# Kernel tuning notes

Hardware: AMD Instinct MI355X
Metric: run time of the kernel (lower is better)

## Reference

```python
import jax, jax.numpy as jnp
from jax import lax
import numpy as np

H = 512
W = 512
SIGMA = 0.1
IN_CH = [3, 66, 64, 64, 32, 32, 32, 16, 16]
OUT_CH = [64, 64, 64, 32, 32, 32, 16, 16, 16]
N_LAYERS = 9


def setup_inputs() -> dict:
    key = jax.random.key(0)
    ks = jax.random.split(key, 32)
    inp = {}
    inp['x'] = jax.random.uniform(ks[0], (3, 3, 1, 1), jnp.float32)  # query + 2 neighbor coords
    inp['neighbors'] = jax.random.uniform(ks[1], (2, 3, H, W), jnp.float32)
    inp['albedo_index'] = 4
    for i in range(N_LAYERS):
        kh = 1 if i == 0 else 3
        fan_in = IN_CH[i] * kh * kh
        inp[f'w{i}'] = jax.random.normal(ks[2 + i], (OUT_CH[i], IN_CH[i], kh, kh), jnp.float32) / np.sqrt(fan_in).astype(np.float32)
        inp[f'b{i}'] = jnp.zeros((OUT_CH[i],), jnp.float32)
    inp['wf'] = jax.random.normal(ks[20], (6, 16, 3, 3), jnp.float32) / np.sqrt(16 * 9).astype(np.float32)
    inp['bf'] = jnp.zeros((6,), jnp.float32)
    inp['albedos'] = 0.5 + jax.random.uniform(ks[21], (9, 3, H, W), jnp.float32)
    return inp


def _conv(x, w, b):
    y = lax.conv_general_dilated(x, w, (1, 1), 'VALID', dimension_numbers=('NCHW', 'OIHW', 'NCHW'))
    return y + b[None, :, None, None]


def _decoder(x, ws, bs, wf, bf):
    # coordconv constant [[ [0,2],[0,2] ], [ [0,0],[2,2] ]] with shape [2,2,2]
    coordconv = jnp.array([[[0., 2.], [0., 2.]], [[0., 0.], [2., 2.]]], dtype=x.dtype)
    for i in range(N_LAYERS):
        x = jnp.repeat(jnp.repeat(x, 2, axis=2), 2, axis=3)  # nearest upsample x2
        if i > 0:
            x = jnp.pad(x, ((0, 0), (0, 0), (1, 1), (1, 1)), mode='reflect')
        x = jax.nn.leaky_relu(_conv(x, ws[i], bs[i]), 0.01)
        if i == 0:
            cc = jnp.broadcast_to(coordconv[None], (x.shape[0],) + coordconv.shape)
            x = jnp.concatenate([x, cc], axis=1)  # -> 66 channels at 2x2
    x = jnp.pad(x, ((0, 0), (0, 0), (1, 1), (1, 1)), mode='reflect')
    return jnp.tanh(_conv(x, wf, bf))  # [B, 6, H, W]


def _grid_sample_border(img, grid):
    # bilinear, padding_mode='border', align_corners=False (matches torch grid_sample)
    N, C, Hh, Ww = img.shape
    gx = jnp.clip((grid[..., 0] + 1.0) * Ww / 2.0 - 0.5, 0.0, Ww - 1.0)
    gy = jnp.clip((grid[..., 1] + 1.0) * Hh / 2.0 - 0.5, 0.0, Hh - 1.0)
    x0 = jnp.floor(gx)
    y0 = jnp.floor(gy)
    wx = (gx - x0)[:, None]  # [N,1,H,W]
    wy = (gy - y0)[:, None]
    x0i = jnp.clip(x0.astype(jnp.int32), 0, Ww - 1)
    x1i = jnp.clip(x0i + 1, 0, Ww - 1)
    y0i = jnp.clip(y0.astype(jnp.int32), 0, Hh - 1)
    y1i = jnp.clip(y0i + 1, 0, Hh - 1)
    g = jax.vmap(lambda im, yi, xi: im[:, yi, xi])
    v00 = g(img, y0i, x0i)
    v01 = g(img, y0i, x1i)
    v10 = g(img, y1i, x0i)
    v11 = g(img, y1i, x1i)
    return v00 * (1 - wx) * (1 - wy) + v01 * wx * (1 - wy) + v10 * (1 - wx) * wy + v11 * wx * wy


def _blending(x, neighbors, flows, albedo):
    eps = 1e-5
    light_flow, view_flow, time_flow = flows[:1, 0:2], flows[:1, 2:4], flows[:1, 4:6]
    lf_n, vf_n, tf_n = flows[1:, 0:2], flows[1:, 2:4], flows[1:, 4:6]
    delta = x[:1] - x[1:]  # [2,3,1,1], broadcasts in place of torch.tile
    dl, dv, dt = delta[:, 0:1], delta[:, 1:2], delta[:, 2:3]
    flag = (jnp.abs(dl) > 0).astype(flows.dtype)
    offset_fwd = dl * light_flow + dv * view_flow + dt * time_flow  # [2,2,H,W]
    shading = flag * neighbors / albedo + (1 - flag) * neighbors
    ys = jnp.linspace(-1.0, 1.0, H)
    xs = jnp.linspace(-1.0, 1.0, W)
    grid_base = jnp.stack(jnp.meshgrid(xs, ys, indexing='xy'), axis=-1)  # [H,W,2], (...,0)=x
    grid = grid_base[None] + offset_fwd.transpose(0, 2, 3, 1)  # [2,H,W,2]
    warped_shading = _grid_sample_border(shading, grid)
    warped_vf = _grid_sample_border(vf_n, grid)
    warped_tf = _grid_sample_border(tf_n, grid)
    warped_lf = _grid_sample_border(lf_n, grid)
    warped_image = flag * warped_shading * albedo + (1 - flag) * warped_shading
    offset_bwd = dl * warped_lf + dv * warped_vf + dt * warped_tf
    dist = jnp.sum(jnp.abs(offset_fwd - offset_bwd), axis=1, keepdims=True)
    weight = jnp.exp(-SIGMA * W * dist)
    wn = weight / (jnp.sum(weight, axis=0, keepdims=True) + eps)
    return jnp.sum(warped_image * wn, axis=0, keepdims=True)  # [1,3,H,W]


def reference(x, neighbors, albedo_index, w0, w1, w2, w3, w4, w5, w6, w7, w8,
              b0, b1, b2, b3, b4, b5, b6, b7, b8, wf, bf, albedos):
    ws = [w0, w1, w2, w3, w4, w5, w6, w7, w8]
    bs = [b0, b1, b2, b3, b4, b5, b6, b7, b8]
    flows = _decoder(x, ws, bs, wf, bf)
    albedo = albedos[albedo_index]  # [3,H,W]
    return _blending(x, neighbors, flows, albedo)
```

## Files before the change

kernel.cpp:

```cpp
#include <hip/hip_runtime.h>
#include <hip/hip_bf16.h>
#include <math.h>


#define HH 512
#define WWI 512
#define HWP (HH*WWI)

__global__ void k_layer0(const float* __restrict__ xin, const float* __restrict__ w,
                         const float* __restrict__ bias, float* __restrict__ out)
{
  for (int idx = threadIdx.x; idx < 3*66*4; idx += blockDim.x) {
    int pos = idx & 3;
    int c = (idx >> 2) % 66;
    int b = idx / (66*4);
    float v;
    if (c < 64) {
      float a = bias[c];
      #pragma unroll
      for (int ci = 0; ci < 3; ci++) a += w[c*3+ci] * xin[b*3+ci];
      v = (a >= 0.f) ? a : 0.01f*a;
    } else {
      int xx = pos & 1, yy = pos >> 1;
      v = (c == 64) ? 2.f*(float)xx : 2.f*(float)yy;
    }
    out[idx] = v;
  }
}

__device__ __forceinline__ int refl_up(int t, int n) {
  t = (t < 0) ? -t : t;
  t = (t >= n) ? (2*(n-1) - t) : t;
  return t >> 1;
}

template<int G>
__global__ void k_conv_lds(const float* __restrict__ in, float* __restrict__ out,
                           const float* __restrict__ w, const float* __restrict__ bias,
                           int B, int Cin, int CO, int COB, int Hin, int TR, int SPAN)
{
  extern __shared__ float lds[];
  const int Hout = Hin * 2;
  const int rowTiles = Hout / TR;
  const int coTiles = CO / COB;
  int bid = blockIdx.x;
  int tile = bid % rowTiles;
  int cot  = (bid / rowTiles) % coTiles;
  int b    = bid / (rowTiles * coTiles);
  int tr0  = tile * TR;
  int co_base = cot * COB;

  int r0 = tr0/2 - 1;
  if (r0 < 0) r0 = 0;
  if (r0 > Hin - SPAN) r0 = Hin - SPAN;

  float* wlds = lds;
  float* blds = wlds + COB*Cin*9;
  float* ilds = blds + COB;

  int nt = blockDim.x, tid = threadIdx.x;

  const float* wsrc = w + (size_t)co_base*Cin*9;
  for (int i = tid; i < COB*Cin*9; i += nt) wlds[i] = wsrc[i];
  for (int i = tid; i < COB; i += nt) blds[i] = bias[co_base + i];
  int icount = Cin*SPAN*Hin;
  for (int i = tid; i < icount; i += nt) {
    int col = i % Hin;
    int r = (i / Hin) % SPAN;
    int ci = i / (Hin*SPAN);
    ilds[i] = in[(((size_t)b*Cin + ci)*Hin + (r0 + r))*Hin + col];
  }
  __syncthreads();

  int npix = TR * Hout;
  int ngr = COB / G;
  int items = ngr * npix;
  for (int it = tid; it < items; it += nt) {
    int pix = it % npix;
    int cg = it / npix;
    int x = pix % Hout;
    int y = tr0 + pix / Hout;

    int ry[3], rx[3];
    #pragma unroll
    for (int d = 0; d < 3; d++) {
      int s = refl_up(y - 1 + d, Hout) - r0;
      s = (s < 0) ? 0 : s;
      s = (s > SPAN-1) ? SPAN-1 : s;
      ry[d] = s;
      rx[d] = refl_up(x - 1 + d, Hout);
    }

    float acc[G];
    #pragma unroll
    for (int j = 0; j < G; j++) acc[j] = blds[cg*G + j];

    for (int ci = 0; ci < Cin; ci++) {
      const float* ib = ilds + (size_t)ci*SPAN*Hin;
      float p[9];
      #pragma unroll
      for (int dy = 0; dy < 3; dy++)
        #pragma unroll
        for (int dx = 0; dx < 3; dx++)
          p[dy*3+dx] = ib[ry[dy]*Hin + rx[dx]];
      const float* wc = wlds + ((size_t)(cg*G)*Cin + ci)*9;
      #pragma unroll
      for (int j = 0; j < G; j++) {
        #pragma unroll
        for (int k = 0; k < 9; k++) acc[j] += wc[(size_t)j*Cin*9 + k] * p[k];
      }
    }

    #pragma unroll
    for (int j = 0; j < G; j++) {
      float v = acc[j];
      v = (v >= 0.f) ? v : 0.01f*v;
      out[(((size_t)b*CO + co_base + cg*G + j)*Hout + y)*Hout + x] = v;
    }
  }
}

__global__ void k_foldw6(const float* __restrict__ w3, const float* __restrict__ w4,
                         const float* __restrict__ w5, const float* __restrict__ w6,
                         const float* __restrict__ w7, const float* __restrict__ w8,
                         float* __restrict__ f3, float* __restrict__ f4,
                         float* __restrict__ f5, float* __restrict__ f6,
                         float* __restrict__ f7, float* __restrict__ f8)
{
  int idx = blockIdx.x*blockDim.x + threadIdx.x;
  const float* w; float* f; int n;
  if      (idx < 2048) { w = w3; f = f3; n = idx; }
  else if (idx < 3072) { w = w4; f = f4; n = idx - 2048; }
  else if (idx < 4096) { w = w5; f = f5; n = idx - 3072; }
  else if (idx < 4608) { w = w6; f = f6; n = idx - 4096; }
  else if (idx < 4864) { w = w7; f = f7; n = idx - 4608; }
  else if (idx < 5120) { w = w8; f = f8; n = idx - 4864; }
  else return;

  const float* ws = w + (size_t)n*9;
  float W[9];
  #pragma unroll
  for (int k = 0; k < 9; k++) W[k] = ws[k];

  float a[2][2][3];
  #pragma unroll
  for (int c = 0; c < 3; c++) {
    a[0][0][c] = W[c];          a[0][1][c] = W[3+c] + W[6+c];
    a[1][0][c] = W[c] + W[3+c]; a[1][1][c] = W[6+c];
  }
  float* fo = f + (size_t)n*16;
  #pragma unroll
  for (int py = 0; py < 2; py++)
    #pragma unroll
    for (int px = 0; px < 2; px++) {
      int p = py*2 + px;
      #pragma unroll
      for (int ky = 0; ky < 2; ky++) {
        float kx0 = (px == 0) ? a[py][ky][0] : (a[py][ky][0] + a[py][ky][1]);
        float kx1 = (px == 0) ? (a[py][ky][1] + a[py][ky][2]) : a[py][ky][2];
        fo[p*4 + ky*2 + 0] = kx0;
        fo[p*4 + ky*2 + 1] = kx1;
      }
    }
}

__global__ void k_upconv_s(const float* __restrict__ in, float* __restrict__ out,
                           const float* __restrict__ wfold, const float* __restrict__ bias,
                           int B, int Cin, int CO, int Hin)
{
  extern __shared__ float4 wlds4[];
  int nt = blockDim.x, tid = threadIdx.x;
  int co = blockIdx.y;
  int stride = Cin + 1;
  const float4* wsrc = reinterpret_cast<const float4*>(wfold);
  for (int s = tid; s < Cin*4; s += nt) {
    int p = s & 3;
    int ci = s >> 2;
    wlds4[p*stride + ci] = wsrc[(size_t)(co*Cin + ci)*4 + p];
  }
  __syncthreads();

  int Hout = Hin * 2;
  int npix = B * Hout * Hout;
  int idx = blockIdx.x*nt + tid;
  if (idx >= npix) return;
  int x = idx % Hout;
  int y = (idx / Hout) % Hout;
  int b = idx / (Hout * Hout);

  int X = x >> 1, Y = y >> 1;
  int px = x & 1, py = y & 1;

  int r_lo = py ? Y : (Y > 0 ? Y-1 : 0);
  int r_hi = py ? (Y < Hin-1 ? Y+1 : Hin-1) : Y;
  int c_lo = px ? X : (X > 0 ? X-1 : 0);
  int c_hi = px ? (X < Hin-1 ? X+1 : Hin-1) : X;

  float acc = bias[co];

  const size_t plane = (size_t)Hin * Hin;
  const float* ibase = in + (size_t)b * Cin * plane;
  const float4* wb = wlds4 + (py*2 + px) * stride;

  for (int ci = 0; ci < Cin; ci++) {
    const float* ip = ibase + (size_t)ci * plane;
    const float* rl = ip + (size_t)r_lo * Hin;
    const float* rh = ip + (size_t)r_hi * Hin;
    float4 w4 = wb[ci];
    acc += w4.x*rl[c_lo] + w4.y*rl[c_hi] + w4.z*rh[c_lo] + w4.w*rh[c_hi];
  }

  float v = (acc >= 0.f) ? acc : 0.01f*acc;
  out[((size_t)b*CO + co)*((size_t)Hout*Hout) + (size_t)y*Hout + x] = v;
}

template<int CO>
__global__ void k_upconv_w(const float* __restrict__ in, float* __restrict__ out,
                           const float* __restrict__ wfold, const float* __restrict__ bias,
                           int B, int Cin, int Hin)
{
  extern __shared__ float4 wlds4[];
  int nt = blockDim.x, tid = threadIdx.x;
  int stride = Cin * CO + 1;
  int nw = Cin * CO * 4;
  const float4* wsrc = reinterpret_cast<const float4*>(wfold);
  for (int s = tid; s < nw; s += nt) {
    int p = s & 3;
    int r = s >> 2;
    int ci = r % Cin;
    int co = r / Cin;
    wlds4[p*stride + ci*CO + co] = wsrc[s];
  }
  __syncthreads();

  int Hout = Hin * 2;
  int total = B * Hout * Hout;
  int idx = blockIdx.x*nt + tid;
  if (idx >= total) return;
  int x = idx % Hout;
  int y = (idx / Hout) % Hout;
  int b = idx / (Hout * Hout);

  int X = x >> 1, Y = y >> 1;
  int px = x & 1, py = y & 1;

  int r_lo = py ? Y : (Y > 0 ? Y-1 : 0);
  int r_hi = py ? (Y < Hin-1 ? Y+1 : Hin-1) : Y;
  int c_lo = px ? X : (X > 0 ? X-1 : 0);
  int c_hi = px ? (X < Hin-1 ? X+1 : Hin-1) : X;

  float acc[CO];
  #pragma unroll
  for (int co = 0; co < CO; co++) acc[co] = bias[co];

  const size_t plane = (size_t)Hin * Hin;
  const float* ibase = in + (size_t)b * Cin * plane;
  const float4* wb = wlds4 + (py*2 + px) * stride;

  for (int ci = 0; ci < Cin; ci++) {
    const float* ip = ibase + (size_t)ci * plane;
    const float* rl = ip + (size_t)r_lo * Hin;
    const float* rh = ip + (size_t)r_hi * Hin;
    float p00 = rl[c_lo], p01 = rl[c_hi];
    float p10 = rh[c_lo], p11 = rh[c_hi];

    const float4* wc = wb + ci * CO;
    #pragma unroll
    for (int co = 0; co < CO; co++) {
      float4 w4 = wc[co];
      acc[co] += w4.x*p00 + w4.y*p01 + w4.z*p10 + w4.w*p11;
    }
  }

  int pix = y*Hout + x;
  #pragma unroll
  for (int co = 0; co < CO; co++) {
    float v = acc[co];
    v = (v >= 0.f) ? v : 0.01f*v;
    out[((size_t)b*CO + co)*((size_t)Hout*Hout) + pix] = v;
  }
}

template<int CO>
__global__ void k_upconv_w2(const float* __restrict__ in, float* __restrict__ out,
                            const float* __restrict__ wfold, const float* __restrict__ bias,
                            int B, int Cin, int Hin)
{
  extern __shared__ float4 wlds4[];
  int nt = blockDim.x, tid = threadIdx.x;
  int stride = Cin * CO + 1;
  int nw = Cin * CO * 4;
  const float4* wsrc = reinterpret_cast<const float4*>(wfold);
  for (int s = tid; s < nw; s += nt) {
    int p = s & 3;
    int r = s >> 2;
    int ci = r % Cin;
    int co = r / Cin;
    wlds4[p*stride + ci*CO + co] = wsrc[s];
  }
  __syncthreads();

  int Hout = Hin * 2;
  int half = Hout >> 1;
  int total = B * Hout * half;
  int idx = blockIdx.x*nt + tid;
  if (idx >= total) return;
  int x1 = idx % half;
  int y  = (idx / half) % Hout;
  int b  = idx / (half * Hout);

  int px = x1 & 1, py = y & 1;
  int X1 = x1 >> 1, Y = y >> 1;
  int X2 = X1 + (Hin >> 1);

  int r_lo = py ? Y : (Y > 0 ? Y-1 : 0);
  int r_hi = py ? (Y < Hin-1 ? Y+1 : Hin-1) : Y;
  int c1lo = px ? X1 : (X1 > 0 ? X1-1 : 0);
  int c1hi = px ? (X1 < Hin-1 ? X1+1 : Hin-1) : X1;
  int c2lo = px ? X2 : (X2 > 0 ? X2-1 : 0);
  int c2hi = px ? (X2 < Hin-1 ? X2+1 : Hin-1) : X2;

  float acc0[CO], acc1[CO];
  #pragma unroll
  for (int co = 0; co < CO; co++) { float bv = bias[co]; acc0[co] = bv; acc1[co] = bv; }

  const size_t plane = (size_t)Hin * Hin;
  const float* ibase = in + (size_t)b * Cin * plane;
  const float4* wb = wlds4 + (py*2 + px) * stride;

  for (int ci = 0; ci < Cin; ci++) {
    const float* ip = ibase + (size_t)ci * plane;
    const float* rl = ip + (size_t)r_lo * Hin;
    const float* rh = ip + (size_t)r_hi * Hin;
    float a0 = rl[c1lo], a1 = rl[c1hi];
    float a2 = rh[c1lo], a3 = rh[c1hi];
    float b0 = rl[c2lo], b1 = rl[c2hi];
    float b2 = rh[c2lo], b3 = rh[c2hi];

    const float4* wc = wb + ci * CO;
    #pragma unroll
    for (int co = 0; co < CO; co++) {
      float4 w4 = wc[co];
      acc0[co] += w4.x*a0 + w4.y*a1 + w4.z*a2 + w4.w*a3;
      acc1[co] += w4.x*b0 + w4.y*b1 + w4.z*b2 + w4.w*b3;
    }
  }

  size_t oplane = (size_t)Hout * Hout;
  size_t pix1 = (size_t)y*Hout + x1;
  float* obase = out + (size_t)b * CO * oplane;
  #pragma unroll
  for (int co = 0; co < CO; co++) {
    float v0 = acc0[co]; v0 = (v0 >= 0.f) ? v0 : 0.01f*v0;
    float v1 = acc1[co]; v1 = (v1 >= 0.f) ? v1 : 0.01f*v1;
    float* op = obase + (size_t)co * oplane;
    op[pix1] = v0;
    op[pix1 + half] = v1;
  }
}

__global__ void k_final(const float* __restrict__ in, float* __restrict__ out,
                        const float* __restrict__ w, const float* __restrict__ bias)
{
  int idx = blockIdx.x*blockDim.x + threadIdx.x;
  int total = 3 * HWP;
  if (idx >= total) return;
  int x = idx & (WWI-1);
  int y = (idx >> 9) & (HH-1);
  int b = idx / HWP;

  int ry[3], rx[3];
  #pragma unroll
  for (int d = 0; d < 3; d++) {
    int t = y - 1 + d;
    t = (t < 0) ? -t : t;
    ry[d] = (t >= HH) ? (2*(HH-1) - t) : t;
    t = x - 1 + d;
    t = (t < 0) ? -t : t;
    rx[d] = (t >= WWI) ? (2*(WWI-1) - t) : t;
  }

  float acc[6];
  #pragma unroll
  for (int co = 0; co < 6; co++) acc[co] = bias[co];

  for (int ci = 0; ci < 16; ci++) {
    const float* ib = in + ((size_t)(b*16) + ci) * HWP;
    float p[9];
    #pragma unroll
    for (int dy = 0; dy < 3; dy++)
      #pragma unroll
      for (int dx = 0; dx < 3; dx++)
        p[dy*3+dx] = ib[ry[dy]*WWI + rx[dx]];
    const float* wc = w + ci*9;
    #pragma unroll
    for (int co = 0; co < 6; co++) {
      const float* wcc = wc + co*16*9;
      #pragma unroll
      for (int k = 0; k < 9; k++) acc[co] += wcc[k] * p[k];
    }
  }

  int pix = y*WWI + x;
  #pragma unroll
  for (int co = 0; co < 6; co++)
    out[((size_t)(b*6) + co)*HWP + pix] = tanhf(acc[co]);
}

__global__ void k_blend(const float* __restrict__ xin, const float* __restrict__ neighbors,
                        const int* __restrict__ aidx, const float* __restrict__ albedos,
                        const float* __restrict__ flows, float* __restrict__ out)
{
  int idx = blockIdx.x*blockDim.x + threadIdx.x;
  if (idx >= HWP) return;
  int xo = idx & (WWI-1);
  int yo = idx >> 9;

  float xv[9];
  #pragma unroll
  for (int i = 0; i < 9; i++) xv[i] = xin[i];

  float f0[6];
  #pragma unroll
  for (int c = 0; c < 6; c++) f0[c] = flows[(size_t)c*HWP + idx];

  const float* alb = albedos + (size_t)aidx[0]*3*HWP;
  float albp[3];
  #pragma unroll
  for (int ch = 0; ch < 3; ch++) albp[ch] = alb[(size_t)ch*HWP + idx];

  float num0 = 0.f, num1 = 0.f, num2 = 0.f;
  float wsum = 0.f;

  #pragma unroll
  for (int n = 0; n < 2; n++) {
    float dl = xv[0] - xv[(n+1)*3 + 0];
    float dv = xv[1] - xv[(n+1)*3 + 1];
    float dt = xv[2] - xv[(n+1)*3 + 2];
    bool fl = fabsf(dl) > 0.f;

    float ofx = dl*f0[0] + dv*f0[2] + dt*f0[4];
    float ofy = dl*f0[1] + dv*f0[3] + dt*f0[5];

    float gx = ((-1.f + (2.f/511.f)*(float)xo) + ofx + 1.f)*256.f - 0.5f;
    float gy = ((-1.f + (2.f/511.f)*(float)yo) + ofy + 1.f)*256.f - 0.5f;
    gx = fminf(fmaxf(gx, 0.f), 511.f);
    gy = fminf(fmaxf(gy, 0.f), 511.f);

    float x0f = floorf(gx), y0f = floorf(gy);
    float wx = gx - x0f, wy = gy - y0f;
    int x0i = (int)x0f, y0i = (int)y0f;
    int x1i = min(x0i + 1, WWI-1), y1i = min(y0i + 1, HH-1);

    float cw[4] = {(1.f-wx)*(1.f-wy), wx*(1.f-wy), (1.f-wx)*wy, wx*wy};
    int   cp[4] = {y0i*WWI + x0i, y0i*WWI + x1i, y1i*WWI + x0i, y1i*WWI + x1i};

    const float* nb = neighbors + (size_t)n*3*HWP;
    const float* Fn = flows + (size_t)(n+1)*6*HWP;

    float s0=0.f,s1=0.f,s2=0.f;
    float l0=0.f,l1=0.f,v0=0.f,v1=0.f,t0=0.f,t1=0.f;
    #pragma unroll
    for (int c = 0; c < 4; c++) {
      int p = cp[c];
      float ww = cw[c];
      float n0 = nb[p];
      float n1 = nb[HWP + p];
      float n2 = nb[2*HWP + p];
      if (fl) {
        n0 /= alb[p];
        n1 /= alb[HWP + p];
        n2 /= alb[2*HWP + p];
      }
      s0 += ww*n0; s1 += ww*n1; s2 += ww*n2;
      l0 += ww*Fn[p];             l1 += ww*Fn[HWP + p];
      v0 += ww*Fn[2*HWP + p];     v1 += ww*Fn[3*HWP + p];
      t0 += ww*Fn[4*HWP + p];     t1 += ww*Fn[5*HWP + p];
    }

    float wi0 = fl ? s0*albp[0] : s0;
    float wi1 = fl ? s1*albp[1] : s1;
    float wi2 = fl ? s2*albp[2] : s2;

    float obx = dl*l0 + dv*v0 + dt*t0;
    float oby = dl*l1 + dv*v1 + dt*t1;
    float dist = fabsf(ofx - obx) + fabsf(ofy - oby);
    float wgt = expf(-51.2f * dist);

    wsum += wgt;
    num0 += wgt*wi0; num1 += wgt*wi1; num2 += wgt*wi2;
  }

  float inv = 1.f / (wsum + 1e-5f);
  out[idx]         = num0*inv;
  out[HWP + idx]   = num1*inv;
  out[2*HWP + idx] = num2*inv;
}

extern "C" void kernel_launch(void* const* d_in, const int* in_sizes, int n_in,
                              void* d_out, int out_size, void* d_ws, size_t ws_size,
                              hipStream_t stream) {
  const float* x         = (const float*)d_in[0];
  const float* neighbors = (const float*)d_in[1];
  const int*   aidx      = (const int*)d_in[2];
  const float* wts[10];
  const float* bis[10];
  for (int i = 0; i < 9; i++) { wts[i] = (const float*)d_in[3+2*i]; bis[i] = (const float*)d_in[4+2*i]; }
  wts[9] = (const float*)d_in[21];
  bis[9] = (const float*)d_in[22];
  const float* albedos = (const float*)d_in[23];

  float* wk   = (float*)d_ws;
  float* bufS = wk;
  float* bufA = wk + 800;
  float* bufB = bufA + 4718592;
  size_t need = (size_t)(800 + 4718592 + 12582912) * 4;
  if (ws_size < need) return;

  float* wf3 = bufA + 3200000;
  float* wf4 = wf3 + 32768;
  float* wf5 = wf4 + 16384;
  float* wf6 = wf5 + 16384;
  float* wf7 = wf6 + 8192;
  float* wf8 = wf7 + 4096;
  k_foldw6<<<20, 256, 0, stream>>>(wts[3], wts[4], wts[5], wts[6], wts[7], wts[8],
                                   wf3, wf4, wf5, wf6, wf7, wf8);

  k_layer0<<<1, 256, 0, stream>>>(x, wts[0], bis[0], bufS);

  auto spanOf = [](int Hin, int TR) { int s = TR/2 + 2; return (s > Hin) ? Hin : s; };
  auto ldsB = [&](int COB, int Cin, int Hin, int TR) {
    return (size_t)(COB*Cin*9 + COB + Cin*spanOf(Hin,TR)*Hin) * 4;
  };

  k_conv_lds<1><<<48, 256, ldsB(4,66,2,4), stream>>>(bufS, bufA, wts[1], bis[1],
                                                     3, 66, 64, 4, 2, 4, spanOf(2,4));
  k_conv_lds<1><<<96, 256, ldsB(2,64,4,8), stream>>>(bufA, bufB, wts[2], bis[2],
                                                     3, 64, 64, 2, 4, 8, spanOf(4,8));
  {
    dim3 g3(3*16*16/256, 32), g4(3*32*32/256, 32), g5(3*64*64/256, 32);
    k_upconv_s<<<g3, 256, (size_t)4*(64+1)*16, stream>>>(bufB, bufA, wf3, bis[3], 3, 64, 32, 8);
    k_upconv_s<<<g4, 256, (size_t)4*(32+1)*16, stream>>>(bufA, bufB, wf4, bis[4], 3, 32, 32, 16);
    k_upconv_s<<<g5, 256, (size_t)4*(32+1)*16, stream>>>(bufB, bufA, wf5, bis[5], 3, 32, 32, 32);
  }

  auto blocks = [](int total){ return (total + 255) / 256; };
  k_upconv_w<16><<<blocks(3*128*128), 256, (size_t)4*(32*16+1)*16, stream>>>(bufA, bufB, wf6, bis[6], 3, 32, 64);
  k_upconv_w2<16><<<blocks(3*256*128), 256, (size_t)4*(16*16+1)*16, stream>>>(bufB, bufA, wf7, bis[7], 3, 16, 128);
  k_upconv_w2<16><<<blocks(3*512*256), 256, (size_t)4*(16*16+1)*16, stream>>>(bufA, bufB, wf8, bis[8], 3, 16, 256);

  k_final<<<blocks(3*HWP), 256, 0, stream>>>(bufB, bufA, wts[9], bis[9]);
  k_blend<<<blocks(HWP), 256, 0, stream>>>(x, neighbors, aidx, albedos, bufA, (float*)d_out);
}
```

Measured before the change: 332.2 us.

## Fold layers 1-2 into upconv, split layer 8 by channel, two-pixel final conv

Layers 1 and 2 now use the same pre-folded 2x2 upsample-conv weights as the later layers, run through the folded small-layer kernel, which removes the generic LDS conv kernel. The layer-8 upconv is split across two output-channel halves per block to cut register pressure and add parallelism. The final 3x3 conv computes two adjacent pixels per thread, sharing the loaded neighbourhood and writing float2. The fold kernel grows to cover eight layers, and the channel split for layer 8 reads each input twice.

Result: faster. 321.2 us (-3.3%).

```diff
diff --git a/kernel.cpp b/kernel.cpp
--- a/kernel.cpp
+++ b/kernel.cpp
@@ -28,113 +28,25 @@
   }
 }
 
-__device__ __forceinline__ int refl_up(int t, int n) {
-  t = (t < 0) ? -t : t;
-  t = (t >= n) ? (2*(n-1) - t) : t;
-  return t >> 1;
-}
-
-template<int G>
-__global__ void k_conv_lds(const float* __restrict__ in, float* __restrict__ out,
-                           const float* __restrict__ w, const float* __restrict__ bias,
-                           int B, int Cin, int CO, int COB, int Hin, int TR, int SPAN)
-{
-  extern __shared__ float lds[];
-  const int Hout = Hin * 2;
-  const int rowTiles = Hout / TR;
-  const int coTiles = CO / COB;
-  int bid = blockIdx.x;
-  int tile = bid % rowTiles;
-  int cot  = (bid / rowTiles) % coTiles;
-  int b    = bid / (rowTiles * coTiles);
-  int tr0  = tile * TR;
-  int co_base = cot * COB;
-
-  int r0 = tr0/2 - 1;
-  if (r0 < 0) r0 = 0;
-  if (r0 > Hin - SPAN) r0 = Hin - SPAN;
-
-  float* wlds = lds;
-  float* blds = wlds + COB*Cin*9;
-  float* ilds = blds + COB;
-
-  int nt = blockDim.x, tid = threadIdx.x;
-
-  const float* wsrc = w + (size_t)co_base*Cin*9;
-  for (int i = tid; i < COB*Cin*9; i += nt) wlds[i] = wsrc[i];
-  for (int i = tid; i < COB; i += nt) blds[i] = bias[co_base + i];
-  int icount = Cin*SPAN*Hin;
-  for (int i = tid; i < icount; i += nt) {
-    int col = i % Hin;
-    int r = (i / Hin) % SPAN;
-    int ci = i / (Hin*SPAN);
-    ilds[i] = in[(((size_t)b*Cin + ci)*Hin + (r0 + r))*Hin + col];
-  }
-  __syncthreads();
-
-  int npix = TR * Hout;
-  int ngr = COB / G;
-  int items = ngr * npix;
-  for (int it = tid; it < items; it += nt) {
-    int pix = it % npix;
-    int cg = it / npix;
-    int x = pix % Hout;
-    int y = tr0 + pix / Hout;
-
-    int ry[3], rx[3];
-    #pragma unroll
-    for (int d = 0; d < 3; d++) {
-      int s = refl_up(y - 1 + d, Hout) - r0;
-      s = (s < 0) ? 0 : s;
-      s = (s > SPAN-1) ? SPAN-1 : s;
-      ry[d] = s;
-      rx[d] = refl_up(x - 1 + d, Hout);
-    }
-
-    float acc[G];
-    #pragma unroll
-    for (int j = 0; j < G; j++) acc[j] = blds[cg*G + j];
-
-    for (int ci = 0; ci < Cin; ci++) {
-      const float* ib = ilds + (size_t)ci*SPAN*Hin;
-      float p[9];
-      #pragma unroll
-      for (int dy = 0; dy < 3; dy++)
-        #pragma unroll
-        for (int dx = 0; dx < 3; dx++)
-          p[dy*3+dx] = ib[ry[dy]*Hin + rx[dx]];
-      const float* wc = wlds + ((size_t)(cg*G)*Cin + ci)*9;
-      #pragma unroll
-      for (int j = 0; j < G; j++) {
-        #pragma unroll
-        for (int k = 0; k < 9; k++) acc[j] += wc[(size_t)j*Cin*9 + k] * p[k];
-      }
-    }
-
-    #pragma unroll
-    for (int j = 0; j < G; j++) {
-      float v = acc[j];
-      v = (v >= 0.f) ? v : 0.01f*v;
-      out[(((size_t)b*CO + co_base + cg*G + j)*Hout + y)*Hout + x] = v;
-    }
-  }
-}
-
-__global__ void k_foldw6(const float* __restrict__ w3, const float* __restrict__ w4,
+__global__ void k_foldw8(const float* __restrict__ w1, const float* __restrict__ w2,
+                         const float* __restrict__ w3, const float* __restrict__ w4,
                          const float* __restrict__ w5, const float* __restrict__ w6,
                          const float* __restrict__ w7, const float* __restrict__ w8,
+                         float* __restrict__ f1, float* __restrict__ f2,
                          float* __restrict__ f3, float* __restrict__ f4,
                          float* __restrict__ f5, float* __restrict__ f6,
                          float* __restrict__ f7, float* __restrict__ f8)
 {
   int idx = blockIdx.x*blockDim.x + threadIdx.x;
   const float* w; float* f; int n;
-  if      (idx < 2048) { w = w3; f = f3; n = idx; }
-  else if (idx < 3072) { w = w4; f = f4; n = idx - 2048; }
-  else if (idx < 4096) { w = w5; f = f5; n = idx - 3072; }
-  else if (idx < 4608) { w = w6; f = f6; n = idx - 4096; }
-  else if (idx < 4864) { w = w7; f = f7; n = idx - 4608; }
-  else if (idx < 5120) { w = w8; f = f8; n = idx - 4864; }
+  if      (idx < 4224)  { w = w1; f = f1; n = idx; }
+  else if (idx < 8320)  { w = w2; f = f2; n = idx - 4224; }
+  else if (idx < 10368) { w = w3; f = f3; n = idx - 8320; }
+  else if (idx < 11392) { w = w4; f = f4; n = idx - 10368; }
+  else if (idx < 12416) { w = w5; f = f5; n = idx - 11392; }
+  else if (idx < 12928) { w = w6; f = f6; n = idx - 12416; }
+  else if (idx < 13184) { w = w7; f = f7; n = idx - 12928; }
+  else if (idx < 13440) { w = w8; f = f8; n = idx - 13184; }
   else return;
 
   const float* ws = w + (size_t)n*9;
@@ -281,22 +193,23 @@
   }
 }
 
-template<int CO>
-__global__ void k_upconv_w2(const float* __restrict__ in, float* __restrict__ out,
-                            const float* __restrict__ wfold, const float* __restrict__ bias,
-                            int B, int Cin, int Hin)
+template<int COB>
+__global__ void k_upconv_w2c(const float* __restrict__ in, float* __restrict__ out,
+                             const float* __restrict__ wfold, const float* __restrict__ bias,
+                             int B, int Cin, int CO, int Hin)
 {
   extern __shared__ float4 wlds4[];
   int nt = blockDim.x, tid = threadIdx.x;
-  int stride = Cin * CO + 1;
-  int nw = Cin * CO * 4;
+  int co0 = blockIdx.y * COB;
+  int stride = Cin * COB + 1;
+  int nw = Cin * COB * 4;
   const float4* wsrc = reinterpret_cast<const float4*>(wfold);
   for (int s = tid; s < nw; s += nt) {
     int p = s & 3;
     int r = s >> 2;
     int ci = r % Cin;
-    int co = r / Cin;
-    wlds4[p*stride + ci*CO + co] = wsrc[s];
+    int col = r / Cin;
+    wlds4[p*stride + ci*COB + col] = wsrc[(size_t)((co0 + col)*Cin + ci)*4 + p];
   }
   __syncthreads();
 
@@ -320,9 +233,9 @@
   int c2lo = px ? X2 : (X2 > 0 ? X2-1 : 0);
   int c2hi = px ? (X2 < Hin-1 ? X2+1 : Hin-1) : X2;
 
-  float acc0[CO], acc1[CO];
-  #pragma unroll
-  for (int co = 0; co < CO; co++) { float bv = bias[co]; acc0[co] = bv; acc1[co] = bv; }
+  float acc0[COB], acc1[COB];
+  #pragma unroll
+  for (int j = 0; j < COB; j++) { float bv = bias[co0 + j]; acc0[j] = bv; acc1[j] = bv; }
 
   const size_t plane = (size_t)Hin * Hin;
   const float* ibase = in + (size_t)b * Cin * plane;
@@ -337,74 +250,87 @@
     float b0 = rl[c2lo], b1 = rl[c2hi];
     float b2 = rh[c2lo], b3 = rh[c2hi];
 
-    const float4* wc = wb + ci * CO;
-    #pragma unroll
-    for (int co = 0; co < CO; co++) {
-      float4 w4 = wc[co];
-      acc0[co] += w4.x*a0 + w4.y*a1 + w4.z*a2 + w4.w*a3;
-      acc1[co] += w4.x*b0 + w4.y*b1 + w4.z*b2 + w4.w*b3;
+    const float4* wc = wb + ci * COB;
+    #pragma unroll
+    for (int j = 0; j < COB; j++) {
+      float4 w4 = wc[j];
+      acc0[j] += w4.x*a0 + w4.y*a1 + w4.z*a2 + w4.w*a3;
+      acc1[j] += w4.x*b0 + w4.y*b1 + w4.z*b2 + w4.w*b3;
     }
   }
 
   size_t oplane = (size_t)Hout * Hout;
   size_t pix1 = (size_t)y*Hout + x1;
-  float* obase = out + (size_t)b * CO * oplane;
-  #pragma unroll
-  for (int co = 0; co < CO; co++) {
-    float v0 = acc0[co]; v0 = (v0 >= 0.f) ? v0 : 0.01f*v0;
-    float v1 = acc1[co]; v1 = (v1 >= 0.f) ? v1 : 0.01f*v1;
-    float* op = obase + (size_t)co * oplane;
+  float* op = out + ((size_t)b * CO + co0) * oplane;
+  #pragma unroll
+  for (int j = 0; j < COB; j++) {
+    float v0 = acc0[j]; v0 = (v0 >= 0.f) ? v0 : 0.01f*v0;
+    float v1 = acc1[j]; v1 = (v1 >= 0.f) ? v1 : 0.01f*v1;
     op[pix1] = v0;
     op[pix1 + half] = v1;
-  }
-}
-
-__global__ void k_final(const float* __restrict__ in, float* __restrict__ out,
-                        const float* __restrict__ w, const float* __restrict__ bias)
+    op += oplane;
+  }
+}
+
+__global__ void k_final2(const float* __restrict__ in, float* __restrict__ out,
+                         const float* __restrict__ w, const float* __restrict__ bias)
 {
   int idx = blockIdx.x*blockDim.x + threadIdx.x;
-  int total = 3 * HWP;
+  int total = 3 * HH * (WWI/2);
   if (idx >= total) return;
-  int x = idx & (WWI-1);
-  int y = (idx >> 9) & (HH-1);
-  int b = idx / HWP;
-
-  int ry[3], rx[3];
+  int xh = idx % (WWI/2);
+  int y  = (idx / (WWI/2)) % HH;
+  int b  = idx / (HH * (WWI/2));
+  int x0 = 2*xh;
+
+  int ry[3];
   #pragma unroll
   for (int d = 0; d < 3; d++) {
     int t = y - 1 + d;
     t = (t < 0) ? -t : t;
     ry[d] = (t >= HH) ? (2*(HH-1) - t) : t;
-    t = x - 1 + d;
-    t = (t < 0) ? -t : t;
-    rx[d] = (t >= WWI) ? (2*(WWI-1) - t) : t;
-  }
-
-  float acc[6];
-  #pragma unroll
-  for (int co = 0; co < 6; co++) acc[co] = bias[co];
+  }
+  int cx[4];
+  cx[0] = (x0 == 0) ? 1 : x0-1;
+  cx[1] = x0;
+  cx[2] = x0+1;
+  cx[3] = (x0+2 >= WWI) ? (2*(WWI-1) - (x0+2)) : x0+2;
+
+  float acc0[6], acc1[6];
+  #pragma unroll
+  for (int co = 0; co < 6; co++) { float bv = bias[co]; acc0[co] = bv; acc1[co] = bv; }
 
   for (int ci = 0; ci < 16; ci++) {
     const float* ib = in + ((size_t)(b*16) + ci) * HWP;
-    float p[9];
-    #pragma unroll
-    for (int dy = 0; dy < 3; dy++)
+    float p[3][4];
+    #pragma unroll
+    for (int dy = 0; dy < 3; dy++) {
+      const float* r = ib + (size_t)ry[dy]*WWI;
       #pragma unroll
-      for (int dx = 0; dx < 3; dx++)
-        p[dy*3+dx] = ib[ry[dy]*WWI + rx[dx]];
+      for (int dx = 0; dx < 4; dx++) p[dy][dx] = r[cx[dx]];
+    }
     const float* wc = w + ci*9;
     #pragma unroll
     for (int co = 0; co < 6; co++) {
       const float* wcc = wc + co*16*9;
       #pragma unroll
-      for (int k = 0; k < 9; k++) acc[co] += wcc[k] * p[k];
-    }
-  }
-
-  int pix = y*WWI + x;
-  #pragma unroll
-  for (int co = 0; co < 6; co++)
-    out[((size_t)(b*6) + co)*HWP + pix] = tanhf(acc[co]);
+      for (int dy = 0; dy < 3; dy++) {
+        #pragma unroll
+        for (int dx = 0; dx < 3; dx++) {
+          float wv = wcc[dy*3+dx];
+          acc0[co] += wv * p[dy][dx];
+          acc1[co] += wv * p[dy][dx+1];
+        }
+      }
+    }
+  }
+
+  size_t pix = (size_t)y*WWI + x0;
+  #pragma unroll
+  for (int co = 0; co < 6; co++) {
+    float2 v = make_float2(tanhf(acc0[co]), tanhf(acc1[co]));
+    *reinterpret_cast<float2*>(out + ((size_t)(b*6) + co)*HWP + pix) = v;
+  }
 }
 
 __global__ void k_blend(const float* __restrict__ xin, const float* __restrict__ neighbors,
@@ -517,38 +443,41 @@
   size_t need = (size_t)(800 + 4718592 + 12582912) * 4;
   if (ws_size < need) return;
 
-  float* wf3 = bufA + 3200000;
+  float* wf1 = bufA + 3200000;
+  float* wf2 = wf1 + 67584;
+  float* wf3 = wf2 + 65536;
   float* wf4 = wf3 + 32768;
   float* wf5 = wf4 + 16384;
   float* wf6 = wf5 + 16384;
   float* wf7 = wf6 + 8192;
   float* wf8 = wf7 + 4096;
-  k_foldw6<<<20, 256, 0, stream>>>(wts[3], wts[4], wts[5], wts[6], wts[7], wts[8],
-                                   wf3, wf4, wf5, wf6, wf7, wf8);
+  k_foldw8<<<53, 256, 0, stream>>>(wts[1], wts[2], wts[3], wts[4], wts[5], wts[6], wts[7], wts[8],
+                                   wf1, wf2, wf3, wf4, wf5, wf6, wf7, wf8);
 
   k_layer0<<<1, 256, 0, stream>>>(x, wts[0], bis[0], bufS);
 
-  auto spanOf = [](int Hin, int TR) { int s = TR/2 + 2; return (s > Hin) ? Hin : s; };
-  auto ldsB = [&](int COB, int Cin, int Hin, int TR) {
-    return (size_t)(COB*Cin*9 + COB + Cin*spanOf(Hin,TR)*Hin) * 4;
-  };
-
-  k_conv_lds<1><<<48, 256, ldsB(4,66,2,4), stream>>>(bufS, bufA, wts[1], bis[1],
-                                                     3, 66, 64, 4, 2, 4, spanOf(2,4));
-  k_conv_lds<1><<<96, 256, ldsB(2,64,4,8), stream>>>(bufA, bufB, wts[2], bis[2],
-                                                     3, 64, 64, 2, 4, 8, spanOf(4,8));
+  auto blocks = [](int total){ return (total + 255) / 256; };
+
   {
-    dim3 g3(3*16*16/256, 32), g4(3*32*32/256, 32), g5(3*64*64/256, 32);
+    dim3 g1(blocks(3*4*4), 64), g2(blocks(3*8*8), 64);
+    dim3 g3(blocks(3*16*16), 32), g4(blocks(3*32*32), 32), g5(blocks(3*64*64), 32);
+    k_upconv_s<<<g1, 256, (size_t)4*(66+1)*16, stream>>>(bufS, bufA, wf1, bis[1], 3, 66, 64, 2);
+    k_upconv_s<<<g2, 256, (size_t)4*(64+1)*16, stream>>>(bufA, bufB, wf2, bis[2], 3, 64, 64, 4);
     k_upconv_s<<<g3, 256, (size_t)4*(64+1)*16, stream>>>(bufB, bufA, wf3, bis[3], 3, 64, 32, 8);
     k_upconv_s<<<g4, 256, (size_t)4*(32+1)*16, stream>>>(bufA, bufB, wf4, bis[4], 3, 32, 32, 16);
     k_upconv_s<<<g5, 256, (size_t)4*(32+1)*16, stream>>>(bufB, bufA, wf5, bis[5], 3, 32, 32, 32);
   }
 
-  auto blocks = [](int total){ return (total + 255) / 256; };
   k_upconv_w<16><<<blocks(3*128*128), 256, (size_t)4*(32*16+1)*16, stream>>>(bufA, bufB, wf6, bis[6], 3, 32, 64);
-  k_upconv_w2<16><<<blocks(3*256*128), 256, (size_t)4*(16*16+1)*16, stream>>>(bufB, bufA, wf7, bis[7], 3, 16, 128);
-  k_upconv_w2<16><<<blocks(3*512*256), 256, (size_t)4*(16*16+1)*16, stream>>>(bufA, bufB, wf8, bis[8], 3, 16, 256);
-
-  k_final<<<blocks(3*HWP), 256, 0, stream>>>(bufB, bufA, wts[9], bis[9]);
+  {
+    dim3 g7(blocks(3*256*128), 1);
+    k_upconv_w2c<16><<<g7, 256, (size_t)4*(16*16+1)*16, stream>>>(bufB, bufA, wf7, bis[7], 3, 16, 16, 128);
+  }
+  {
+    dim3 g8(blocks(3*512*256), 2);
+    k_upconv_w2c<8><<<g8, 256, (size_t)4*(16*8+1)*16, stream>>>(bufA, bufB, wf8, bis[8], 3, 16, 16, 256);
+  }
+
+  k_final2<<<blocks(3*HH*(WWI/2)), 256, 0, stream>>>(bufB, bufA, wts[9], bis[9]);
   k_blend<<<blocks(HWP), 256, 0, stream>>>(x, neighbors, aidx, albedos, bufA, (float*)d_out);
 }
```
